# Optimization experiments

Hardware: AMD Instinct MI355X
Metric: run time of the kernel (lower is better)

The kernel has to match this reference:

```python
import jax, jax.numpy as jnp
import numpy as np

IN_FEATURES = 8192
OUT_FEATURES = 8192
BATCH = 64


def setup_inputs() -> dict:
    key = jax.random.key(0)
    k_x, k_mu = jax.random.split(key)
    x = jax.random.normal(k_x, (BATCH, IN_FEATURES), dtype=jnp.float32)
    # torch init: mu = rand(in,1) * out_features; sigma = ones*10; amplitude = ones; bias = zeros
    mu = jax.random.uniform(k_mu, (IN_FEATURES, 1), dtype=jnp.float32) * OUT_FEATURES
    sigma = jnp.ones((IN_FEATURES, 1), dtype=jnp.float32) * 10.0
    amplitude = jnp.ones((IN_FEATURES, 1), dtype=jnp.float32)
    bias = jnp.zeros((OUT_FEATURES,), dtype=jnp.float32)
    return {"x": x, "mu": mu, "sigma": sigma, "amplitude": amplitude, "bias": bias}


def reference(x, mu, sigma, amplitude, bias):
    out_features = bias.shape[0]
    positions = jnp.arange(out_features, dtype=x.dtype)[None, :]  # [1, out]
    diff = positions - mu                                          # [in, out]
    weight = amplitude * jnp.exp(-(diff * diff) / (2.0 * sigma * sigma))  # [in, out]
    out = x @ weight                                               # [B, out]
    return jax.nn.relu(out + bias)
```

## Files before the change

### kernel.cpp

```cpp
#include <hip/hip_runtime.h>

#define IN_F 8192
#define OUT_F 8192
#define BATCH 64
#define PASS 2048
#define TQ 32
#define ROWS 16
#define CH 64

__global__ __launch_bounds__(256) void transpose_x_kern(const float* __restrict__ x,
                                                        float* __restrict__ xT) {
    __shared__ float tile[64][65];
    const int i0 = blockIdx.x * 64;
    const int tid = threadIdx.x;
#pragma unroll
    for (int u = tid; u < 64 * 64; u += 256) {
        const int b = u >> 6;
        const int i = u & 63;
        tile[i][b] = x[b * IN_F + i0 + i];
    }
    __syncthreads();
#pragma unroll
    for (int u = tid; u < 64 * 64; u += 256) {
        const int i = u >> 6;
        const int b = u & 63;
        xT[(i0 + i) * 64 + b] = tile[i][b];
    }
}

__global__ __launch_bounds__(256, 4) void gauss_fc_kern(
    const float* __restrict__ x, const float* __restrict__ xT,
    const float4* __restrict__ mu4, const float4* __restrict__ sg4,
    const float* __restrict__ amp, const float* __restrict__ bias,
    float* __restrict__ out, const int use_xt) {

    __shared__ float lmu[PASS];
    __shared__ float lk[PASS];
    __shared__ float lamp[PASS];
    __shared__ int   li[PASS];
    __shared__ float xs[CH][ROWS];
    __shared__ int   cnt;

    const int tid = threadIdx.x;
    const int c = tid & 31;
    const int g = tid >> 5;
    const int tile0 = blockIdx.x * TQ;
    const int row0 = blockIdx.y * ROWS;
    const float colf = (float)(tile0 + c);
    const float lo = (float)tile0;
    const float hi = (float)(tile0 + TQ - 1);

    float acc0 = 0.f, acc1 = 0.f;

    for (int base = 0; base < IN_F; base += PASS) {
        if (tid == 0) cnt = 0;
        __syncthreads();

        const int q_end = (base + PASS) >> 2;
        for (int q = (base >> 2) + tid; q < q_end; q += 256) {
            const float4 m4 = mu4[q];
            const float4 s4 = sg4[q];
            const float ms[4] = {m4.x, m4.y, m4.z, m4.w};
            const float ss[4] = {s4.x, s4.y, s4.z, s4.w};
#pragma unroll
            for (int e = 0; e < 4; ++e) {
                const float m = ms[e];
                const float s = ss[e];
                const float R = 8.0f * fabsf(s) + 1.0f;
                if (m >= lo - R && m <= hi + R) {
                    const int i = (q << 2) + e;
                    const int p = atomicAdd(&cnt, 1);
                    lmu[p] = m;
                    lk[p] = -0.5f / (s * s);
                    lamp[p] = amp[i];
                    li[p] = i;
                }
            }
        }
        __syncthreads();
        const int n = cnt;

        for (int cb = 0; cb < n; cb += CH) {
            const int cn = min(CH, n - cb);
            for (int u = tid; u < (cn << 4); u += 256) {
                const int ci = u >> 4;
                const int r = u & 15;
                const int i = li[cb + ci];
                xs[ci][r] = use_xt ? xT[i * 64 + row0 + r]
                                   : x[(size_t)(row0 + r) * IN_F + i];
            }
            __syncthreads();

            const int g2 = g << 1;
#pragma unroll 4
            for (int j = 0; j < cn; ++j) {
                const float d = colf - lmu[cb + j];
                const float w = lamp[cb + j] * __expf(lk[cb + j] * d * d);
                acc0 += w * xs[j][g2 + 0];
                acc1 += w * xs[j][g2 + 1];
            }
            __syncthreads();
        }
    }

    const float bb = bias[tile0 + c];
    const int r0 = row0 + (g << 1);
    const float v0 = acc0 + bb;
    const float v1 = acc1 + bb;
    out[(size_t)r0 * OUT_F + tile0 + c]       = v0 > 0.f ? v0 : 0.f;
    out[(size_t)(r0 + 1) * OUT_F + tile0 + c] = v1 > 0.f ? v1 : 0.f;
}

extern "C" void kernel_launch(void* const* d_in, const int* in_sizes, int n_in,
                              void* d_out, int out_size, void* d_ws, size_t ws_size,
                              hipStream_t stream) {
    const float* x     = (const float*)d_in[0];
    const float* mu    = (const float*)d_in[1];
    const float* sigma = (const float*)d_in[2];
    const float* amp   = (const float*)d_in[3];
    const float* bias  = (const float*)d_in[4];
    float* out = (float*)d_out;

    const size_t xt_bytes = (size_t)IN_F * BATCH * sizeof(float);
    const int use_xt = (ws_size >= xt_bytes) ? 1 : 0;
    float* xT = (float*)d_ws;

    if (use_xt) {
        transpose_x_kern<<<IN_F / 64, 256, 0, stream>>>(x, xT);
    }
    dim3 grid(OUT_F / TQ, BATCH / ROWS);
    gauss_fc_kern<<<grid, 256, 0, stream>>>(x, xT,
                                            (const float4*)mu, (const float4*)sigma,
                                            amp, bias, out, use_xt);
}
```

Before: 95.90 us.

## Bin Gaussian inputs into per-tile global lists instead of per-block scanning

A new prep kernel bins each input feature into per-output-tile lists in workspace using global atomics. It also does the x transpose in the same launch. The main kernel then reads only the relevant packed (mu,k,amp,idx) entries and loads x rows as float4. This removes the redundant full scan of all 8192 mu/sigma values by every block. It costs an extra zero kernel and atomic contention, and assumes the workspace is large enough. Entries beyond the capacity are silently dropped.

```diff
diff --git a/kernel.cpp b/kernel.cpp
--- a/kernel.cpp
+++ b/kernel.cpp
@@ -3,104 +3,108 @@
 #define IN_F 8192
 #define OUT_F 8192
 #define BATCH 64
-#define PASS 2048
 #define TQ 32
-#define ROWS 16
-#define CH 64
+#define NT (OUT_F / TQ)
+#define CAP_MAX 2048
+#define CH 256
+#define CNT_STRIDE 16
 
-__global__ __launch_bounds__(256) void transpose_x_kern(const float* __restrict__ x,
-                                                        float* __restrict__ xT) {
-    __shared__ float tile[64][65];
-    const int i0 = blockIdx.x * 64;
+#define XT_BYTES ((size_t)IN_F * BATCH * 4)
+#define CNT_OFF  XT_BYTES
+#define CNT_BYTES ((size_t)NT * CNT_STRIDE * 4)
+#define ENT_OFF  (CNT_OFF + CNT_BYTES)
+
+__global__ __launch_bounds__(256) void zero_cnt_kern(int* __restrict__ cnt) {
     const int tid = threadIdx.x;
 #pragma unroll
-    for (int u = tid; u < 64 * 64; u += 256) {
-        const int b = u >> 6;
-        const int i = u & 63;
-        tile[i][b] = x[b * IN_F + i0 + i];
-    }
-    __syncthreads();
+    for (int u = tid; u < NT * CNT_STRIDE; u += 256) cnt[u] = 0;
+}
+
+__global__ __launch_bounds__(256) void prep_kern(
+    const float* __restrict__ x, float* __restrict__ xT,
+    const float* __restrict__ mu, const float* __restrict__ sigma,
+    const float* __restrict__ amp,
+    int* __restrict__ cnt, float4* __restrict__ ent, const int cap) {
+
+    const int tid = threadIdx.x;
+    if (blockIdx.x < 128) {
+        __shared__ float tile[64][65];
+        const int i0 = blockIdx.x * 64;
 #pragma unroll
-    for (int u = tid; u < 64 * 64; u += 256) {
-        const int i = u >> 6;
-        const int b = u & 63;
-        xT[(i0 + i) * 64 + b] = tile[i][b];
+        for (int u = tid; u < 64 * 64; u += 256) {
+            const int b = u >> 6;
+            const int i = u & 63;
+            tile[i][b] = x[b * IN_F + i0 + i];
+        }
+        __syncthreads();
+#pragma unroll
+        for (int u = tid; u < 64 * 64; u += 256) {
+            const int i = u >> 6;
+            const int b = u & 63;
+            xT[(i0 + i) * 64 + b] = tile[i][b];
+        }
+    } else {
+        const int i = (blockIdx.x - 128) * 256 + tid;
+        const float m = mu[i];
+        const float s = sigma[i];
+        const float a = amp[i];
+        const float R = 8.0f * fabsf(s) + 1.0f;
+        const float k = -0.5f / (s * s);
+        int t_lo = (int)floorf((m - R - (float)(TQ - 1)) * (1.0f / TQ));
+        int t_hi = (int)floorf((m + R) * (1.0f / TQ)) + 1;
+        t_lo = max(t_lo, 0);
+        t_hi = min(t_hi, NT - 1);
+        const float4 e = make_float4(m, k, a, __int_as_float(i));
+        for (int t = t_lo; t <= t_hi; ++t) {
+            const int p = atomicAdd(&cnt[t * CNT_STRIDE], 1);
+            if (p < cap) ent[(size_t)t * cap + p] = e;
+        }
     }
 }
 
 __global__ __launch_bounds__(256, 4) void gauss_fc_kern(
-    const float* __restrict__ x, const float* __restrict__ xT,
-    const float4* __restrict__ mu4, const float4* __restrict__ sg4,
-    const float* __restrict__ amp, const float* __restrict__ bias,
-    float* __restrict__ out, const int use_xt) {
+    const float* __restrict__ xT, const int* __restrict__ cnt,
+    const float4* __restrict__ ent, const float* __restrict__ bias,
+    float* __restrict__ out, const int cap) {
 
-    __shared__ float lmu[PASS];
-    __shared__ float lk[PASS];
-    __shared__ float lamp[PASS];
-    __shared__ int   li[PASS];
-    __shared__ float xs[CH][ROWS];
-    __shared__ int   cnt;
+    __shared__ float4 es[CH];
+    __shared__ float xs[CH][16];
 
     const int tid = threadIdx.x;
     const int c = tid & 31;
     const int g = tid >> 5;
-    const int tile0 = blockIdx.x * TQ;
-    const int row0 = blockIdx.y * ROWS;
+    const int t = blockIdx.x;
+    const int row0 = blockIdx.y * 16;
+    const int tile0 = t * TQ;
     const float colf = (float)(tile0 + c);
-    const float lo = (float)tile0;
-    const float hi = (float)(tile0 + TQ - 1);
+    const int n = min(cnt[t * CNT_STRIDE], cap);
+    const float4* lst = ent + (size_t)t * cap;
 
     float acc0 = 0.f, acc1 = 0.f;
 
-    for (int base = 0; base < IN_F; base += PASS) {
-        if (tid == 0) cnt = 0;
+    for (int cb = 0; cb < n; cb += CH) {
+        const int cn = min(CH, n - cb);
+        if (tid < cn) es[tid] = lst[cb + tid];
+        __syncthreads();
+        for (int u = tid; u < (cn << 2); u += 256) {
+            const int ci = u >> 2;
+            const int rq = (u & 3) << 2;
+            const int i = __float_as_int(es[ci].w);
+            const float4 v = *(const float4*)&xT[i * 64 + row0 + rq];
+            *(float4*)&xs[ci][rq] = v;
+        }
         __syncthreads();
 
-        const int q_end = (base + PASS) >> 2;
-        for (int q = (base >> 2) + tid; q < q_end; q += 256) {
-            const float4 m4 = mu4[q];
-            const float4 s4 = sg4[q];
-            const float ms[4] = {m4.x, m4.y, m4.z, m4.w};
-            const float ss[4] = {s4.x, s4.y, s4.z, s4.w};
-#pragma unroll
-            for (int e = 0; e < 4; ++e) {
-                const float m = ms[e];
-                const float s = ss[e];
-                const float R = 8.0f * fabsf(s) + 1.0f;
-                if (m >= lo - R && m <= hi + R) {
-                    const int i = (q << 2) + e;
-                    const int p = atomicAdd(&cnt, 1);
-                    lmu[p] = m;
-                    lk[p] = -0.5f / (s * s);
-                    lamp[p] = amp[i];
-                    li[p] = i;
-                }
-            }
+        const int g2 = g << 1;
+#pragma unroll 4
+        for (int j = 0; j < cn; ++j) {
+            const float4 e = es[j];
+            const float d = colf - e.x;
+            const float w = e.z * __expf(e.y * d * d);
+            acc0 += w * xs[j][g2 + 0];
+            acc1 += w * xs[j][g2 + 1];
         }
         __syncthreads();
-        const int n = cnt;
-
-        for (int cb = 0; cb < n; cb += CH) {
-            const int cn = min(CH, n - cb);
-            for (int u = tid; u < (cn << 4); u += 256) {
-                const int ci = u >> 4;
-                const int r = u & 15;
-                const int i = li[cb + ci];
-                xs[ci][r] = use_xt ? xT[i * 64 + row0 + r]
-                                   : x[(size_t)(row0 + r) * IN_F + i];
-            }
-            __syncthreads();
-
-            const int g2 = g << 1;
-#pragma unroll 4
-            for (int j = 0; j < cn; ++j) {
-                const float d = colf - lmu[cb + j];
-                const float w = lamp[cb + j] * __expf(lk[cb + j] * d * d);
-                acc0 += w * xs[j][g2 + 0];
-                acc1 += w * xs[j][g2 + 1];
-            }
-            __syncthreads();
-        }
     }
 
     const float bb = bias[tile0 + c];
@@ -121,15 +125,20 @@
     const float* bias  = (const float*)d_in[4];
     float* out = (float*)d_out;
 
-    const size_t xt_bytes = (size_t)IN_F * BATCH * sizeof(float);
-    const int use_xt = (ws_size >= xt_bytes) ? 1 : 0;
-    float* xT = (float*)d_ws;
+    char* ws = (char*)d_ws;
+    float*  xT      = (float*)ws;
+    int*    tileCnt = (int*)(ws + CNT_OFF);
+    float4* ent     = (float4*)(ws + ENT_OFF);
 
-    if (use_xt) {
-        transpose_x_kern<<<IN_F / 64, 256, 0, stream>>>(x, xT);
+    int cap = CAP_MAX;
+    if (ws_size < ENT_OFF + (size_t)NT * CAP_MAX * sizeof(float4)) {
+        const size_t avail = (ws_size > ENT_OFF) ? (ws_size - ENT_OFF) : 0;
+        cap = (int)(avail / ((size_t)NT * sizeof(float4)));
+        if (cap < 1) cap = 1;
     }
-    dim3 grid(OUT_F / TQ, BATCH / ROWS);
-    gauss_fc_kern<<<grid, 256, 0, stream>>>(x, xT,
-                                            (const float4*)mu, (const float4*)sigma,
-                                            amp, bias, out, use_xt);
+
+    zero_cnt_kern<<<1, 256, 0, stream>>>(tileCnt);
+    prep_kern<<<160, 256, 0, stream>>>(x, xT, mu, sigma, amp, tileCnt, ent, cap);
+    dim3 grid(NT, BATCH / 16);
+    gauss_fc_kern<<<grid, 256, 0, stream>>>(xT, tileCnt, ent, bias, out, cap);
 }
```

After: 104.8 us. +9.3%, slower.

## Precompute Gaussian weight tile in shared memory and widen column tile

Applied to the files above, without the earlier changes.

Doubles the output column tile to 64 and precomputes each chunk's Gaussian weights once into a shared weight tile using exp2f with a folded log2e constant. The inner loop then becomes pure FMAs over four accumulators instead of recomputing exp per row pair. The candidate list is packed into float4 entries and x rows are loaded with float4 vectors. Each block does more work, but the grid now has half as many blocks, occupancy is lowered to 2 blocks per SM, and the mu scan is redundant across fewer tiles.

```diff
diff --git a/kernel.cpp b/kernel.cpp
--- a/kernel.cpp
+++ b/kernel.cpp
@@ -3,9 +3,10 @@
 #define IN_F 8192
 #define OUT_F 8192
 #define BATCH 64
+#define TQ 64
+#define NTILE (OUT_F / TQ)
+#define ROWS 16
 #define PASS 2048
-#define TQ 32
-#define ROWS 16
 #define CH 64
 
 __global__ __launch_bounds__(256) void transpose_x_kern(const float* __restrict__ x,
@@ -28,29 +29,27 @@
     }
 }
 
-__global__ __launch_bounds__(256, 4) void gauss_fc_kern(
+__global__ __launch_bounds__(256, 2) void gauss_fc_kern(
     const float* __restrict__ x, const float* __restrict__ xT,
     const float4* __restrict__ mu4, const float4* __restrict__ sg4,
     const float* __restrict__ amp, const float* __restrict__ bias,
     float* __restrict__ out, const int use_xt) {
 
-    __shared__ float lmu[PASS];
-    __shared__ float lk[PASS];
-    __shared__ float lamp[PASS];
-    __shared__ int   li[PASS];
-    __shared__ float xs[CH][ROWS];
+    __shared__ float4 list[PASS];
+    __shared__ float wtile[CH][64];
+    __shared__ float xtile[CH][ROWS];
     __shared__ int   cnt;
 
     const int tid = threadIdx.x;
     const int c = tid & 31;
     const int g = tid >> 5;
+    const int g2 = g << 1;
     const int tile0 = blockIdx.x * TQ;
     const int row0 = blockIdx.y * ROWS;
-    const float colf = (float)(tile0 + c);
     const float lo = (float)tile0;
     const float hi = (float)(tile0 + TQ - 1);
 
-    float acc0 = 0.f, acc1 = 0.f;
+    float acc00 = 0.f, acc01 = 0.f, acc10 = 0.f, acc11 = 0.f;
 
     for (int base = 0; base < IN_F; base += PASS) {
         if (tid == 0) cnt = 0;
@@ -70,10 +69,8 @@
                 if (m >= lo - R && m <= hi + R) {
                     const int i = (q << 2) + e;
                     const int p = atomicAdd(&cnt, 1);
-                    lmu[p] = m;
-                    lk[p] = -0.5f / (s * s);
-                    lamp[p] = amp[i];
-                    li[p] = i;
+                    list[p] = make_float4(m, -0.72134752f / (s * s), amp[i],
+                                          __int_as_float(i));
                 }
             }
         }
@@ -82,33 +79,54 @@
 
         for (int cb = 0; cb < n; cb += CH) {
             const int cn = min(CH, n - cb);
-            for (int u = tid; u < (cn << 4); u += 256) {
-                const int ci = u >> 4;
-                const int r = u & 15;
-                const int i = li[cb + ci];
-                xs[ci][r] = use_xt ? xT[i * 64 + row0 + r]
-                                   : x[(size_t)(row0 + r) * IN_F + i];
+
+            for (int u = tid; u < (cn << 6); u += 256) {
+                const int j = u >> 6;
+                const int cc = u & 63;
+                const float4 e = list[cb + j];
+                const float d = (float)(tile0 + cc) - e.x;
+                wtile[j][cc] = e.z * exp2f(e.y * d * d);
+            }
+            {
+                const int ci = tid >> 2;
+                const int rq = (tid & 3) << 2;
+                if (ci < cn) {
+                    const int i = __float_as_int(list[cb + ci].w);
+                    if (use_xt) {
+                        *(float4*)&xtile[ci][rq] = *(const float4*)&xT[i * 64 + row0 + rq];
+                    } else {
+                        xtile[ci][rq + 0] = x[(size_t)(row0 + rq + 0) * IN_F + i];
+                        xtile[ci][rq + 1] = x[(size_t)(row0 + rq + 1) * IN_F + i];
+                        xtile[ci][rq + 2] = x[(size_t)(row0 + rq + 2) * IN_F + i];
+                        xtile[ci][rq + 3] = x[(size_t)(row0 + rq + 3) * IN_F + i];
+                    }
+                }
             }
             __syncthreads();
 
-            const int g2 = g << 1;
-#pragma unroll 4
+#pragma unroll 8
             for (int j = 0; j < cn; ++j) {
-                const float d = colf - lmu[cb + j];
-                const float w = lamp[cb + j] * __expf(lk[cb + j] * d * d);
-                acc0 += w * xs[j][g2 + 0];
-                acc1 += w * xs[j][g2 + 1];
+                const float w0 = wtile[j][c];
+                const float w1 = wtile[j][c + 32];
+                const float2 xv = *(const float2*)&xtile[j][g2];
+                acc00 += w0 * xv.x;
+                acc01 += w0 * xv.y;
+                acc10 += w1 * xv.x;
+                acc11 += w1 * xv.y;
             }
             __syncthreads();
         }
     }
 
-    const float bb = bias[tile0 + c];
-    const int r0 = row0 + (g << 1);
-    const float v0 = acc0 + bb;
-    const float v1 = acc1 + bb;
-    out[(size_t)r0 * OUT_F + tile0 + c]       = v0 > 0.f ? v0 : 0.f;
-    out[(size_t)(r0 + 1) * OUT_F + tile0 + c] = v1 > 0.f ? v1 : 0.f;
+    const float b0 = bias[tile0 + c];
+    const float b1 = bias[tile0 + c + 32];
+    const int r0 = row0 + g2;
+    float* o0 = out + (size_t)r0 * OUT_F + tile0 + c;
+    float* o1 = o0 + OUT_F;
+    o0[0]  = fmaxf(acc00 + b0, 0.f);
+    o1[0]  = fmaxf(acc01 + b0, 0.f);
+    o0[32] = fmaxf(acc10 + b1, 0.f);
+    o1[32] = fmaxf(acc11 + b1, 0.f);
 }
 
 extern "C" void kernel_launch(void* const* d_in, const int* in_sizes, int n_in,
@@ -128,7 +146,7 @@
     if (use_xt) {
         transpose_x_kern<<<IN_F / 64, 256, 0, stream>>>(x, xT);
     }
-    dim3 grid(OUT_F / TQ, BATCH / ROWS);
+    dim3 grid(NTILE, BATCH / ROWS);
     gauss_fc_kern<<<grid, 256, 0, stream>>>(x, xT,
                                             (const float4*)mu, (const float4*)sigma,
                                             amp, bias, out, use_xt);
```

Result: faster. 91.97 us (-4.1%).
